# Kernel tuning notes

Hardware: AMD Instinct MI355X
Metric: run time of the kernel (lower is better)

Reference implementation:

```python
import jax, jax.numpy as jnp
import numpy as np

N_HEADS = 16
D_MODEL = 1024
D_HEAD = D_MODEL // N_HEADS


def setup_inputs() -> dict:
    key = jax.random.key(0)
    k1, k2, k3 = jax.random.split(key, 3)
    b, t, d = 2, 2048, D_MODEL
    x = jax.random.normal(k1, (b, t, d), dtype=jnp.float32)
    # Linear weights stored as [in, out] so y = x @ W (equivalent to torch's x @ W.T)
    w_qkv = jax.random.normal(k2, (d, 3 * d), dtype=jnp.float32) * (1.0 / np.sqrt(d))
    w_out = jax.random.normal(k3, (d, d), dtype=jnp.float32) * (1.0 / np.sqrt(d))
    return {"x": x, "w_qkv": w_qkv, "w_out": w_out}


def reference(x, w_qkv, w_out):
    b, t, d = x.shape
    h, dh = N_HEADS, D_HEAD
    qkv = x @ w_qkv                                   # (b, t, 3d)
    q, k, v = jnp.split(qkv, 3, axis=-1)
    # (b, h, t, dh)
    q = q.reshape(b, t, h, dh).transpose(0, 2, 1, 3)
    k = k.reshape(b, t, h, dh).transpose(0, 2, 1, 3)
    v = v.reshape(b, t, h, dh).transpose(0, 2, 1, 3)
    scale = 1.0 / np.sqrt(dh).astype(np.float32)
    att = jnp.einsum('bhqd,bhkd->bhqk', q, k) * scale  # (b, h, t, t)
    causal = jnp.tril(jnp.ones((t, t), dtype=bool))
    att = jnp.where(causal, att, -jnp.inf)
    att = jax.nn.softmax(att, axis=-1)
    y = jnp.einsum('bhqk,bhkd->bhqd', att, v)          # (b, h, t, dh)
    y = y.transpose(0, 2, 1, 3).reshape(b, t, d)
    return y @ w_out
```

## Files before the change

kernel.cpp:

```cpp
#include <hip/hip_runtime.h>
#include <hip/hip_bf16.h>
#include <stdint.h>

typedef __bf16 bf16x8 __attribute__((ext_vector_type(8)));
typedef float  f32x4  __attribute__((ext_vector_type(4)));

#define B_   2
#define T_   2048
#define H_   16
#define DH_  64
#define DM_  1024
#define BH_  (B_*H_)
#define M_   (B_*T_)

#define QSCALE 0.18033688f
#define FIXED_M 8.0f

#define SBAR() __builtin_amdgcn_sched_barrier(0)

static __device__ __forceinline__ void gload_lds16(const void* g, void* lds) {
  __builtin_amdgcn_global_load_lds(
      (const __attribute__((address_space(1))) void*)(uintptr_t)g,
      (__attribute__((address_space(3))) void*)(uint32_t)(uintptr_t)lds,
      16, 0, 0);
}

__global__ void k_prep(const float* __restrict__ x, const float* __restrict__ wqkv,
                       const float* __restrict__ wout, __hip_bfloat16* __restrict__ xb,
                       __hip_bfloat16* __restrict__ wqkvT, __hip_bfloat16* __restrict__ woutT) {
  __shared__ float tile[32][33];
  const int bid = blockIdx.x, tid = threadIdx.x;
  if (bid < 4096) {
    int i = bid * 256 + tid;
    float4 v = reinterpret_cast<const float4*>(x)[i];
    alignas(8) __hip_bfloat16 t[4] = {__float2bfloat16(v.x), __float2bfloat16(v.y),
                                      __float2bfloat16(v.z), __float2bfloat16(v.w)};
    reinterpret_cast<uint2*>(xb)[i] = *reinterpret_cast<const uint2*>(t);
    return;
  }
  const float* in; __hip_bfloat16* out; int K, N, n0, k0;
  if (bid < 7168) {
    int t = bid - 4096; in = wqkv; out = wqkvT; K = 1024; N = 3072;
    n0 = (t % 96) * 32; k0 = (t / 96) * 32;
  } else {
    int t = bid - 7168; in = wout; out = woutT; K = 1024; N = 1024;
    n0 = (t % 32) * 32; k0 = (t / 32) * 32;
  }
  int kl = tid >> 3, n4 = (tid & 7) * 4;
  float4 v = *reinterpret_cast<const float4*>(in + (size_t)(k0 + kl) * N + n0 + n4);
  tile[kl][n4 + 0] = v.x; tile[kl][n4 + 1] = v.y; tile[kl][n4 + 2] = v.z; tile[kl][n4 + 3] = v.w;
  __syncthreads();
  int nl = tid >> 3, k4 = (tid & 7) * 4;
  alignas(8) __hip_bfloat16 t[4];
  #pragma unroll
  for (int j = 0; j < 4; ++j) t[j] = __float2bfloat16(tile[k4 + j][nl]);
  *reinterpret_cast<uint2*>(out + (size_t)(n0 + nl) * K + k0 + k4) = *reinterpret_cast<const uint2*>(t);
}

template<int BM, int BN, int FM, int FN>
static __device__ __forceinline__ void gemm_core_pipe(
    const __hip_bfloat16* __restrict__ A, const __hip_bfloat16* __restrict__ BT,
    int K, int brow, int bcol, __hip_bfloat16* As, __hip_bfloat16* Bs,
    f32x4 acc[FM][FN]) {
  constexpr int WGN = BN / (16 * FN);
  constexpr int LOADS = BM / 64 + BN / 64;
  constexpr int ASLOT = BM * 32, BSLOT = BN * 32;
  const int tid = threadIdx.x, wave = tid >> 6, lane = tid & 63;
  const int wr = wave / WGN, wc = wave % WGN;
  const int llo = lane & 15, lhi = lane >> 4;
  const int nk = K / 32;
  const int schunk = (lane & 3) ^ ((lane >> 3) & 3);
  auto stage = [&](int ks, int slot) {
    #pragma unroll
    for (int c = wave; c < BM / 16; c += 4)
      gload_lds16(A + (size_t)(brow + c * 16 + (lane >> 2)) * K + ks * 32 + schunk * 8,
                  As + slot * ASLOT + c * 512);
    #pragma unroll
    for (int c = wave; c < BN / 16; c += 4)
      gload_lds16(BT + (size_t)(bcol + c * 16 + (lane >> 2)) * K + ks * 32 + schunk * 8,
                  Bs + slot * BSLOT + c * 512);
  };
  stage(0, 0);
  stage(1, 1);
  const int rchunk = lhi ^ ((llo >> 1) & 3);
  for (int ks = 0; ks < nk; ++ks) {
    if constexpr (LOADS == 4)      asm volatile("s_waitcnt vmcnt(4)" ::: "memory");
    else if constexpr (LOADS == 3) asm volatile("s_waitcnt vmcnt(3)" ::: "memory");
    else                           asm volatile("s_waitcnt vmcnt(0)" ::: "memory");
    SBAR();
    __builtin_amdgcn_s_barrier();
    SBAR();
    const int s2 = (ks + 2 < nk) ? ks + 2 : nk - 1;
    stage(s2, (ks + 2) % 3);
    const __hip_bfloat16* Asl = As + (ks % 3) * ASLOT;
    const __hip_bfloat16* Bsl = Bs + (ks % 3) * BSLOT;
    bf16x8 a[FM], b[FN];
    #pragma unroll
    for (int i = 0; i < FM; ++i)
      a[i] = *reinterpret_cast<const bf16x8*>(
          Asl + (wr * FM * 16 + i * 16 + llo) * 32 + rchunk * 8);
    #pragma unroll
    for (int j = 0; j < FN; ++j)
      b[j] = *reinterpret_cast<const bf16x8*>(
          Bsl + (wc * FN * 16 + j * 16 + llo) * 32 + rchunk * 8);
    __builtin_amdgcn_s_setprio(1);
    #pragma unroll
    for (int i = 0; i < FM; ++i)
      #pragma unroll
      for (int j = 0; j < FN; ++j)
        acc[i][j] = __builtin_amdgcn_mfma_f32_16x16x32_bf16(a[i], b[j], acc[i][j], 0, 0, 0);
    __builtin_amdgcn_s_setprio(0);
  }
  asm volatile("s_waitcnt vmcnt(0)" ::: "memory");
}

__global__ __launch_bounds__(256) void k_gemm_qkv(
    const __hip_bfloat16* __restrict__ A, const __hip_bfloat16* __restrict__ BT,
    __hip_bfloat16* __restrict__ q_ws, __hip_bfloat16* __restrict__ k_ws,
    __hip_bfloat16* __restrict__ vT) {
  alignas(16) __shared__ __hip_bfloat16 As[3 * 128 * 32];
  alignas(16) __shared__ __hip_bfloat16 Bs[3 * 128 * 32];
  f32x4 acc[4][4] = {};
  const int brow = blockIdx.y * 128, bcol = blockIdx.x * 128;
  gemm_core_pipe<128, 128, 4, 4>(A, BT, DM_, brow, bcol, As, Bs, acc);
  const int tid = threadIdx.x, wave = tid >> 6, lane = tid & 63;
  const int wr = wave >> 1, wc = wave & 1;
  const int llo = lane & 15, lhi = lane >> 4;
  #pragma unroll
  for (int i = 0; i < 4; ++i) {
    const int tbase = brow + wr * 64 + i * 16 + lhi * 4;
    const int b = tbase >> 11, t = tbase & 2047;
    #pragma unroll
    for (int j = 0; j < 4; ++j) {
      int n = bcol + wc * 64 + j * 16 + llo;
      int part = n >> 10, rem = n & 1023, hh = rem >> 6, dh = rem & 63;
      if (part == 2) {
        alignas(8) __hip_bfloat16 tv[4];
        #pragma unroll
        for (int r = 0; r < 4; ++r) tv[r] = __float2bfloat16(acc[i][j][r]);
        *reinterpret_cast<uint2*>(
            vT + (((size_t)(b * H_ + hh)) * DH_ + dh) * T_ + t) =
            *reinterpret_cast<const uint2*>(tv);
      } else {
        float sc = (part == 0) ? QSCALE : 1.0f;
        __hip_bfloat16* dst = (part == 0) ? q_ws : k_ws;
        #pragma unroll
        for (int r = 0; r < 4; ++r)
          dst[(((size_t)(b * H_ + hh)) * T_ + t + r) * DH_ + dh] =
              __float2bfloat16(acc[i][j][r] * sc);
      }
    }
  }
}

__global__ __launch_bounds__(256) void k_gemm_out(
    const __hip_bfloat16* __restrict__ A, const __hip_bfloat16* __restrict__ BT,
    float* __restrict__ C) {
  alignas(16) __shared__ __hip_bfloat16 As[3 * 128 * 32];
  alignas(16) __shared__ __hip_bfloat16 Bs[3 * 64 * 32];
  f32x4 acc[4][2] = {};
  const int brow = blockIdx.y * 128, bcol = blockIdx.x * 64;
  gemm_core_pipe<128, 64, 4, 2>(A, BT, DM_, brow, bcol, As, Bs, acc);
  const int tid = threadIdx.x, wave = tid >> 6, lane = tid & 63;
  const int wr = wave >> 1, wc = wave & 1;
  const int llo = lane & 15, lhi = lane >> 4;
  #pragma unroll
  for (int i = 0; i < 4; ++i)
    #pragma unroll
    for (int j = 0; j < 2; ++j) {
      int n = bcol + wc * 32 + j * 16 + llo;
      #pragma unroll
      for (int r = 0; r < 4; ++r) {
        int m = brow + wr * 64 + i * 16 + lhi * 4 + r;
        C[(size_t)m * DM_ + n] = acc[i][j][r];
      }
    }
}

__global__ __launch_bounds__(512) void k_attn(
    const __hip_bfloat16* __restrict__ Q, const __hip_bfloat16* __restrict__ Kk,
    const __hip_bfloat16* __restrict__ VT, __hip_bfloat16* __restrict__ Y) {
  alignas(16) __shared__ __hip_bfloat16 Ks[4][64 * 64];
  alignas(16) __shared__ __hip_bfloat16 Vs[4][64 * 64];
  alignas(16) __shared__ __hip_bfloat16 Ps[8][16 * 64];
  const int bh = blockIdx.y;
  const int p  = blockIdx.x;
  const int tid = threadIdx.x, wave = tid >> 6, lane = tid & 63;
  const int llo = lane & 15, lhi = lane >> 4;
  const int qt   = (wave < 4) ? (31 - p) : p;
  const int myNt = qt + 1;
  const int ntA  = 32 - p;
  const int q0 = qt * 64;
  const int qbase = q0 + (wave & 3) * 16;
  const int myq = qbase + llo;

  const __hip_bfloat16* kb = Kk + (size_t)bh * T_ * DH_;
  const __hip_bfloat16* vb = VT + (size_t)bh * DH_ * T_;

  const int srow = lane >> 3;
  const int schunk = (lane & 7) ^ srow;
  const int rb = wave * 8;

  bf16x8 aq[2];
  #pragma unroll
  for (int k0 = 0; k0 < 2; ++k0)
    aq[k0] = *reinterpret_cast<const bf16x8*>(
        Q + ((size_t)bh * T_ + myq) * DH_ + k0 * 32 + lhi * 8);

  float lsum = 0.f;
  f32x4 o[4] = {};

  gload_lds16(kb + (size_t)(rb + srow) * DH_ + schunk * 8, &Ks[0][rb * 64]);
  gload_lds16(vb + (size_t)(rb + srow) * T_ + schunk * 8, &Vs[0][rb * 64]);
  gload_lds16(kb + (size_t)(64 + rb + srow) * DH_ + schunk * 8, &Ks[1][rb * 64]);
  gload_lds16(vb + (size_t)(rb + srow) * T_ + 64 + schunk * 8, &Vs[1][rb * 64]);

  char* psw = reinterpret_cast<char*>(&Ps[wave][0]);

  for (int it = 0; it < ntA; ++it) {
    const int cur = it & 3;
    {
      const int ts = (it + 2 < ntA) ? (it + 2) : (ntA - 1);
      const int bs = (it + 2) & 3;
      const int tn = ts * 64;
      gload_lds16(kb + (size_t)(tn + rb + srow) * DH_ + schunk * 8, &Ks[bs][rb * 64]);
      gload_lds16(vb + (size_t)(rb + srow) * T_ + tn + schunk * 8, &Vs[bs][rb * 64]);
    }
    asm volatile("s_waitcnt vmcnt(4)" ::: "memory");
    SBAR();
    __builtin_amdgcn_s_barrier();
    SBAR();

    if (it < myNt) {
      const __hip_bfloat16* ksb = Ks[cur];
      const __hip_bfloat16* vsb = Vs[cur];

      f32x4 s[4];
      __builtin_amdgcn_s_setprio(1);
      #pragma unroll
      for (int jn = 0; jn < 4; ++jn) {
        const __hip_bfloat16* krow = ksb + (jn * 16 + llo) * 64;
        bf16x8 b0 = *reinterpret_cast<const bf16x8*>(krow + ((lhi ^ (llo & 7)) << 3));
        bf16x8 b1 = *reinterpret_cast<const bf16x8*>(krow + (((4 + lhi) ^ (llo & 7)) << 3));
        f32x4 z = {};
        z = __builtin_amdgcn_mfma_f32_16x16x32_bf16(b0, aq[0], z, 0, 0, 0);
        z = __builtin_amdgcn_mfma_f32_16x16x32_bf16(b1, aq[1], z, 0, 0, 0);
        s[jn] = z;
      }
      __builtin_amdgcn_s_setprio(0);
      if (it == myNt - 1) {
        #pragma unroll
        for (int jn = 0; jn < 4; ++jn)
          #pragma unroll
          for (int r = 0; r < 4; ++r) {
            int tprime = q0 + jn * 16 + lhi * 4 + r;
            if (tprime > myq) s[jn][r] = -INFINITY;
          }
      }
      #pragma unroll
      for (int jn = 0; jn < 4; ++jn) {
        float p0 = __builtin_amdgcn_exp2f(s[jn][0] - FIXED_M);
        float p1 = __builtin_amdgcn_exp2f(s[jn][1] - FIXED_M);
        float p2 = __builtin_amdgcn_exp2f(s[jn][2] - FIXED_M);
        float p3 = __builtin_amdgcn_exp2f(s[jn][3] - FIXED_M);
        lsum += (p0 + p1) + (p2 + p3);
        alignas(8) __hip_bfloat16 hp[4] = {
            __float2bfloat16(p0), __float2bfloat16(p1),
            __float2bfloat16(p2), __float2bfloat16(p3)};
        int wbyte = llo * 128 + ((((jn << 1) | (lhi >> 1)) ^ (llo & 7)) << 4) + ((lhi & 1) << 3);
        *reinterpret_cast<uint2*>(psw + wbyte) = *reinterpret_cast<const uint2*>(hp);
      }
      asm volatile("" ::: "memory");
      bf16x8 ap0 = *reinterpret_cast<const bf16x8*>(
          &Ps[wave][llo * 64 + ((lhi ^ (llo & 7)) << 3)]);
      bf16x8 ap1 = *reinterpret_cast<const bf16x8*>(
          &Ps[wave][llo * 64 + (((4 + lhi) ^ (llo & 7)) << 3)]);
      __builtin_amdgcn_s_setprio(1);
      #pragma unroll
      for (int jd = 0; jd < 4; ++jd) {
        const __hip_bfloat16* vrow = vsb + (jd * 16 + llo) * 64;
        bf16x8 v0 = *reinterpret_cast<const bf16x8*>(vrow + ((lhi ^ (llo & 7)) << 3));
        bf16x8 v1 = *reinterpret_cast<const bf16x8*>(vrow + (((4 + lhi) ^ (llo & 7)) << 3));
        o[jd] = __builtin_amdgcn_mfma_f32_16x16x32_bf16(v0, ap0, o[jd], 0, 0, 0);
        o[jd] = __builtin_amdgcn_mfma_f32_16x16x32_bf16(v1, ap1, o[jd], 0, 0, 0);
      }
      __builtin_amdgcn_s_setprio(0);
    }
  }

  lsum += __shfl_xor(lsum, 16);
  lsum += __shfl_xor(lsum, 32);
  const float inv = 1.0f / lsum;

  const int b = bh >> 4, h = bh & 15;
  __hip_bfloat16* yrow = Y + ((size_t)(b * T_ + myq)) * DM_ + h * 64;
  #pragma unroll
  for (int jd = 0; jd < 4; ++jd) {
    alignas(8) __hip_bfloat16 t4[4];
    #pragma unroll
    for (int r = 0; r < 4; ++r) t4[r] = __float2bfloat16(o[jd][r] * inv);
    *reinterpret_cast<uint2*>(yrow + jd * 16 + lhi * 4) =
        *reinterpret_cast<const uint2*>(t4);
  }
}

extern "C" void kernel_launch(void* const* d_in, const int* in_sizes, int n_in,
                              void* d_out, int out_size, void* d_ws, size_t ws_size,
                              hipStream_t stream) {
  const float* x     = (const float*)d_in[0];
  const float* w_qkv = (const float*)d_in[1];
  const float* w_out = (const float*)d_in[2];
  float* out = (float*)d_out;
  char* ws = (char*)d_ws;

  size_t off = 0;
  __hip_bfloat16* xb    = (__hip_bfloat16*)(ws + off); off += (size_t)M_ * DM_ * 2;
  __hip_bfloat16* wqkvT = (__hip_bfloat16*)(ws + off); off += (size_t)3 * DM_ * DM_ * 2;
  __hip_bfloat16* woutT = (__hip_bfloat16*)(ws + off); off += (size_t)DM_ * DM_ * 2;
  __hip_bfloat16* q_ws  = (__hip_bfloat16*)(ws + off); off += (size_t)M_ * DM_ * 2;
  __hip_bfloat16* k_ws  = (__hip_bfloat16*)(ws + off); off += (size_t)M_ * DM_ * 2;
  __hip_bfloat16* vT    = (__hip_bfloat16*)(ws + off); off += (size_t)M_ * DM_ * 2;
  __hip_bfloat16* y_ws  = (__hip_bfloat16*)(ws + off); off += (size_t)M_ * DM_ * 2;
  (void)ws_size; (void)in_sizes; (void)n_in; (void)out_size;

  k_prep<<<8192, 256, 0, stream>>>(x, w_qkv, w_out, xb, wqkvT, woutT);

  k_gemm_qkv<<<dim3(3 * DM_ / 128, M_ / 128), 256, 0, stream>>>(xb, wqkvT, q_ws, k_ws, vT);

  k_attn<<<dim3(T_ / 128, BH_), 512, 0, stream>>>(q_ws, k_ws, vT, y_ws);

  k_gemm_out<<<dim3(DM_ / 64, M_ / 128), 256, 0, stream>>>(y_ws, woutT, out);
}
```

Before: 99.68 us.

## Process both paired query tiles per wave sharing K/V fragments, halve block size

Each attention block now uses 4 waves instead of 8, and each wave handles two query rows: one from the high tile and one from the paired low tile. K and V fragments read from LDS are reused across both, which cuts LDS reads per unit of MFMA work. The K/V pipeline shrinks from a 4-slot ring to double buffering with a full __syncthreads per iteration, and LDS footprint falls. Per-wave register pressure rises and parallelism within a block drops, and the simpler pipeline may expose more memory latency.

```diff
diff --git a/kernel.cpp b/kernel.cpp
--- a/kernel.cpp
+++ b/kernel.cpp
@@ -177,93 +177,143 @@
     }
 }
 
-__global__ __launch_bounds__(512) void k_attn(
+__global__ __launch_bounds__(256) void k_attn(
     const __hip_bfloat16* __restrict__ Q, const __hip_bfloat16* __restrict__ Kk,
     const __hip_bfloat16* __restrict__ VT, __hip_bfloat16* __restrict__ Y) {
-  alignas(16) __shared__ __hip_bfloat16 Ks[4][64 * 64];
-  alignas(16) __shared__ __hip_bfloat16 Vs[4][64 * 64];
-  alignas(16) __shared__ __hip_bfloat16 Ps[8][16 * 64];
+  alignas(16) __shared__ __hip_bfloat16 Ks[2][64 * 64];
+  alignas(16) __shared__ __hip_bfloat16 Vs[2][64 * 64];
+  alignas(16) __shared__ __hip_bfloat16 Ps[4][16 * 64];
   const int bh = blockIdx.y;
   const int p  = blockIdx.x;
   const int tid = threadIdx.x, wave = tid >> 6, lane = tid & 63;
   const int llo = lane & 15, lhi = lane >> 4;
-  const int qt   = (wave < 4) ? (31 - p) : p;
-  const int myNt = qt + 1;
-  const int ntA  = 32 - p;
-  const int q0 = qt * 64;
-  const int qbase = q0 + (wave & 3) * 16;
-  const int myq = qbase + llo;
+  const int ntA = 32 - p;
+  const int qhi0 = (31 - p) * 64, qlo0 = p * 64;
+  const int myq_hi = qhi0 + wave * 16 + llo;
+  const int myq_lo = qlo0 + wave * 16 + llo;
 
   const __hip_bfloat16* kb = Kk + (size_t)bh * T_ * DH_;
   const __hip_bfloat16* vb = VT + (size_t)bh * DH_ * T_;
 
   const int srow = lane >> 3;
   const int schunk = (lane & 7) ^ srow;
-  const int rb = wave * 8;
-
-  bf16x8 aq[2];
-  #pragma unroll
-  for (int k0 = 0; k0 < 2; ++k0)
-    aq[k0] = *reinterpret_cast<const bf16x8*>(
-        Q + ((size_t)bh * T_ + myq) * DH_ + k0 * 32 + lhi * 8);
-
-  float lsum = 0.f;
-  f32x4 o[4] = {};
-
-  gload_lds16(kb + (size_t)(rb + srow) * DH_ + schunk * 8, &Ks[0][rb * 64]);
-  gload_lds16(vb + (size_t)(rb + srow) * T_ + schunk * 8, &Vs[0][rb * 64]);
-  gload_lds16(kb + (size_t)(64 + rb + srow) * DH_ + schunk * 8, &Ks[1][rb * 64]);
-  gload_lds16(vb + (size_t)(rb + srow) * T_ + 64 + schunk * 8, &Vs[1][rb * 64]);
+  const int rb = wave * 16;
+
+  bf16x8 aq_hi[2], aq_lo[2];
+  #pragma unroll
+  for (int k0 = 0; k0 < 2; ++k0) {
+    aq_hi[k0] = *reinterpret_cast<const bf16x8*>(
+        Q + ((size_t)bh * T_ + myq_hi) * DH_ + k0 * 32 + lhi * 8);
+    aq_lo[k0] = *reinterpret_cast<const bf16x8*>(
+        Q + ((size_t)bh * T_ + myq_lo) * DH_ + k0 * 32 + lhi * 8);
+  }
+
+  float lsum_hi = 0.f, lsum_lo = 0.f;
+  f32x4 o_hi[4] = {}, o_lo[4] = {};
+
+  auto stage = [&](int tile, int slot) {
+    #pragma unroll
+    for (int g = 0; g < 2; ++g) {
+      const int row = rb + g * 8;
+      gload_lds16(kb + (size_t)(tile * 64 + row + srow) * DH_ + schunk * 8,
+                  &Ks[slot][row * 64]);
+      gload_lds16(vb + (size_t)(row + srow) * T_ + tile * 64 + schunk * 8,
+                  &Vs[slot][row * 64]);
+    }
+  };
+
+  stage(0, 0);
+  __syncthreads();
 
   char* psw = reinterpret_cast<char*>(&Ps[wave][0]);
 
   for (int it = 0; it < ntA; ++it) {
-    const int cur = it & 3;
+    const int cur = it & 1;
+    if (it + 1 < ntA) stage(it + 1, cur ^ 1);
+    const __hip_bfloat16* ksb = Ks[cur];
+    const __hip_bfloat16* vsb = Vs[cur];
+    const bool actlo = (it <= p);
+
+    f32x4 shi[4], slo[4];
+    __builtin_amdgcn_s_setprio(1);
+    #pragma unroll
+    for (int jn = 0; jn < 4; ++jn) {
+      const __hip_bfloat16* krow = ksb + (jn * 16 + llo) * 64;
+      bf16x8 b0 = *reinterpret_cast<const bf16x8*>(krow + ((lhi ^ (llo & 7)) << 3));
+      bf16x8 b1 = *reinterpret_cast<const bf16x8*>(krow + (((4 + lhi) ^ (llo & 7)) << 3));
+      f32x4 z = {};
+      z = __builtin_amdgcn_mfma_f32_16x16x32_bf16(b0, aq_hi[0], z, 0, 0, 0);
+      z = __builtin_amdgcn_mfma_f32_16x16x32_bf16(b1, aq_hi[1], z, 0, 0, 0);
+      shi[jn] = z;
+      if (actlo) {
+        f32x4 w = {};
+        w = __builtin_amdgcn_mfma_f32_16x16x32_bf16(b0, aq_lo[0], w, 0, 0, 0);
+        w = __builtin_amdgcn_mfma_f32_16x16x32_bf16(b1, aq_lo[1], w, 0, 0, 0);
+        slo[jn] = w;
+      }
+    }
+    __builtin_amdgcn_s_setprio(0);
+    if (it == ntA - 1) {
+      #pragma unroll
+      for (int jn = 0; jn < 4; ++jn)
+        #pragma unroll
+        for (int r = 0; r < 4; ++r) {
+          int tprime = qhi0 + jn * 16 + lhi * 4 + r;
+          if (tprime > myq_hi) shi[jn][r] = -INFINITY;
+        }
+    }
+    if (actlo && it == p) {
+      #pragma unroll
+      for (int jn = 0; jn < 4; ++jn)
+        #pragma unroll
+        for (int r = 0; r < 4; ++r) {
+          int tprime = qlo0 + jn * 16 + lhi * 4 + r;
+          if (tprime > myq_lo) slo[jn][r] = -INFINITY;
+        }
+    }
+    bf16x8 vf0[4], vf1[4];
+    #pragma unroll
+    for (int jd = 0; jd < 4; ++jd) {
+      const __hip_bfloat16* vrow = vsb + (jd * 16 + llo) * 64;
+      vf0[jd] = *reinterpret_cast<const bf16x8*>(vrow + ((lhi ^ (llo & 7)) << 3));
+      vf1[jd] = *reinterpret_cast<const bf16x8*>(vrow + (((4 + lhi) ^ (llo & 7)) << 3));
+    }
+    #pragma unroll
+    for (int jn = 0; jn < 4; ++jn) {
+      float p0 = __builtin_amdgcn_exp2f(shi[jn][0] - FIXED_M);
+      float p1 = __builtin_amdgcn_exp2f(shi[jn][1] - FIXED_M);
+      float p2 = __builtin_amdgcn_exp2f(shi[jn][2] - FIXED_M);
+      float p3 = __builtin_amdgcn_exp2f(shi[jn][3] - FIXED_M);
+      lsum_hi += (p0 + p1) + (p2 + p3);
+      alignas(8) __hip_bfloat16 hp[4] = {
+          __float2bfloat16(p0), __float2bfloat16(p1),
+          __float2bfloat16(p2), __float2bfloat16(p3)};
+      int wbyte = llo * 128 + ((((jn << 1) | (lhi >> 1)) ^ (llo & 7)) << 4) + ((lhi & 1) << 3);
+      *reinterpret_cast<uint2*>(psw + wbyte) = *reinterpret_cast<const uint2*>(hp);
+    }
+    asm volatile("" ::: "memory");
     {
-      const int ts = (it + 2 < ntA) ? (it + 2) : (ntA - 1);
-      const int bs = (it + 2) & 3;
-      const int tn = ts * 64;
-      gload_lds16(kb + (size_t)(tn + rb + srow) * DH_ + schunk * 8, &Ks[bs][rb * 64]);
-      gload_lds16(vb + (size_t)(rb + srow) * T_ + tn + schunk * 8, &Vs[bs][rb * 64]);
-    }
-    asm volatile("s_waitcnt vmcnt(4)" ::: "memory");
-    SBAR();
-    __builtin_amdgcn_s_barrier();
-    SBAR();
-
-    if (it < myNt) {
-      const __hip_bfloat16* ksb = Ks[cur];
-      const __hip_bfloat16* vsb = Vs[cur];
-
-      f32x4 s[4];
+      bf16x8 ap0 = *reinterpret_cast<const bf16x8*>(
+          &Ps[wave][llo * 64 + ((lhi ^ (llo & 7)) << 3)]);
+      bf16x8 ap1 = *reinterpret_cast<const bf16x8*>(
+          &Ps[wave][llo * 64 + (((4 + lhi) ^ (llo & 7)) << 3)]);
       __builtin_amdgcn_s_setprio(1);
       #pragma unroll
+      for (int jd = 0; jd < 4; ++jd) {
+        o_hi[jd] = __builtin_amdgcn_mfma_f32_16x16x32_bf16(vf0[jd], ap0, o_hi[jd], 0, 0, 0);
+        o_hi[jd] = __builtin_amdgcn_mfma_f32_16x16x32_bf16(vf1[jd], ap1, o_hi[jd], 0, 0, 0);
+      }
+      __builtin_amdgcn_s_setprio(0);
+    }
+    if (actlo) {
+      asm volatile("" ::: "memory");
+      #pragma unroll
       for (int jn = 0; jn < 4; ++jn) {
-        const __hip_bfloat16* krow = ksb + (jn * 16 + llo) * 64;
-        bf16x8 b0 = *reinterpret_cast<const bf16x8*>(krow + ((lhi ^ (llo & 7)) << 3));
-        bf16x8 b1 = *reinterpret_cast<const bf16x8*>(krow + (((4 + lhi) ^ (llo & 7)) << 3));
-        f32x4 z = {};
-        z = __builtin_amdgcn_mfma_f32_16x16x32_bf16(b0, aq[0], z, 0, 0, 0);
-        z = __builtin_amdgcn_mfma_f32_16x16x32_bf16(b1, aq[1], z, 0, 0, 0);
-        s[jn] = z;
-      }
-      __builtin_amdgcn_s_setprio(0);
-      if (it == myNt - 1) {
-        #pragma unroll
-        for (int jn = 0; jn < 4; ++jn)
-          #pragma unroll
-          for (int r = 0; r < 4; ++r) {
-            int tprime = q0 + jn * 16 + lhi * 4 + r;
-            if (tprime > myq) s[jn][r] = -INFINITY;
-          }
-      }
-      #pragma unroll
-      for (int jn = 0; jn < 4; ++jn) {
-        float p0 = __builtin_amdgcn_exp2f(s[jn][0] - FIXED_M);
-        float p1 = __builtin_amdgcn_exp2f(s[jn][1] - FIXED_M);
-        float p2 = __builtin_amdgcn_exp2f(s[jn][2] - FIXED_M);
-        float p3 = __builtin_amdgcn_exp2f(s[jn][3] - FIXED_M);
-        lsum += (p0 + p1) + (p2 + p3);
+        float p0 = __builtin_amdgcn_exp2f(slo[jn][0] - FIXED_M);
+        float p1 = __builtin_amdgcn_exp2f(slo[jn][1] - FIXED_M);
+        float p2 = __builtin_amdgcn_exp2f(slo[jn][2] - FIXED_M);
+        float p3 = __builtin_amdgcn_exp2f(slo[jn][3] - FIXED_M);
+        lsum_lo += (p0 + p1) + (p2 + p3);
         alignas(8) __hip_bfloat16 hp[4] = {
             __float2bfloat16(p0), __float2bfloat16(p1),
             __float2bfloat16(p2), __float2bfloat16(p3)};
@@ -278,29 +328,36 @@
       __builtin_amdgcn_s_setprio(1);
       #pragma unroll
       for (int jd = 0; jd < 4; ++jd) {
-        const __hip_bfloat16* vrow = vsb + (jd * 16 + llo) * 64;
-        bf16x8 v0 = *reinterpret_cast<const bf16x8*>(vrow + ((lhi ^ (llo & 7)) << 3));
-        bf16x8 v1 = *reinterpret_cast<const bf16x8*>(vrow + (((4 + lhi) ^ (llo & 7)) << 3));
-        o[jd] = __builtin_amdgcn_mfma_f32_16x16x32_bf16(v0, ap0, o[jd], 0, 0, 0);
-        o[jd] = __builtin_amdgcn_mfma_f32_16x16x32_bf16(v1, ap1, o[jd], 0, 0, 0);
+        o_lo[jd] = __builtin_amdgcn_mfma_f32_16x16x32_bf16(vf0[jd], ap0, o_lo[jd], 0, 0, 0);
+        o_lo[jd] = __builtin_amdgcn_mfma_f32_16x16x32_bf16(vf1[jd], ap1, o_lo[jd], 0, 0, 0);
       }
       __builtin_amdgcn_s_setprio(0);
     }
-  }
-
-  lsum += __shfl_xor(lsum, 16);
-  lsum += __shfl_xor(lsum, 32);
-  const float inv = 1.0f / lsum;
+    __syncthreads();
+  }
+
+  lsum_hi += __shfl_xor(lsum_hi, 16);
+  lsum_hi += __shfl_xor(lsum_hi, 32);
+  lsum_lo += __shfl_xor(lsum_lo, 16);
+  lsum_lo += __shfl_xor(lsum_lo, 32);
+  const float inv_hi = 1.0f / lsum_hi;
+  const float inv_lo = 1.0f / lsum_lo;
 
   const int b = bh >> 4, h = bh & 15;
-  __hip_bfloat16* yrow = Y + ((size_t)(b * T_ + myq)) * DM_ + h * 64;
+  __hip_bfloat16* yhi = Y + ((size_t)(b * T_ + myq_hi)) * DM_ + h * 64;
+  __hip_bfloat16* ylo = Y + ((size_t)(b * T_ + myq_lo)) * DM_ + h * 64;
   #pragma unroll
   for (int jd = 0; jd < 4; ++jd) {
     alignas(8) __hip_bfloat16 t4[4];
     #pragma unroll
-    for (int r = 0; r < 4; ++r) t4[r] = __float2bfloat16(o[jd][r] * inv);
-    *reinterpret_cast<uint2*>(yrow + jd * 16 + lhi * 4) =
+    for (int r = 0; r < 4; ++r) t4[r] = __float2bfloat16(o_hi[jd][r] * inv_hi);
+    *reinterpret_cast<uint2*>(yhi + jd * 16 + lhi * 4) =
         *reinterpret_cast<const uint2*>(t4);
+    alignas(8) __hip_bfloat16 t5[4];
+    #pragma unroll
+    for (int r = 0; r < 4; ++r) t5[r] = __float2bfloat16(o_lo[jd][r] * inv_lo);
+    *reinterpret_cast<uint2*>(ylo + jd * 16 + lhi * 4) =
+        *reinterpret_cast<const uint2*>(t5);
   }
 }
 
@@ -327,7 +384,7 @@
 
   k_gemm_qkv<<<dim3(3 * DM_ / 128, M_ / 128), 256, 0, stream>>>(xb, wqkvT, q_ws, k_ws, vT);
 
-  k_attn<<<dim3(T_ / 128, BH_), 512, 0, stream>>>(q_ws, k_ws, vT, y_ws);
+  k_attn<<<dim3(16, BH_), 256, 0, stream>>>(q_ws, k_ws, vT, y_ws);
 
   k_gemm_out<<<dim3(DM_ / 64, M_ / 128), 256, 0, stream>>>(y_ws, woutT, out);
 }
```

Result: slower. 105.2 us (+5.5%).
